# Kernel tuning notes

Hardware: AMD Instinct MI355X
Metric: run time of the kernel (lower is better)

Reference implementation:

```python
import jax, jax.numpy as jnp
import numpy as np

N = 100000      # nodes
E = 1600000     # edges (avg degree 16)
EL = 200000     # supervision (label) edges
D_IN, D_HID, D_OUT = 128, 128, 64


def setup_inputs() -> dict:
    key = jax.random.key(0)
    k = jax.random.split(key, 6)
    x = jax.random.normal(k[0], (N, D_IN), jnp.float32)
    edge_index = jax.random.randint(k[1], (2, E), 0, N, dtype=jnp.int32)
    edge_label_index = jax.random.randint(k[2], (2, EL), 0, N, dtype=jnp.int32)
    W1 = jax.random.normal(k[3], (D_IN, D_HID), jnp.float32) * (1.0 / np.sqrt(D_IN))
    b1 = jnp.zeros((D_HID,), jnp.float32)
    W2 = jax.random.normal(k[4], (D_HID, D_OUT), jnp.float32) * (1.0 / np.sqrt(D_HID))
    b2 = jnp.zeros((D_OUT,), jnp.float32)
    return {"x": x, "edge_index": edge_index, "edge_label_index": edge_label_index,
            "W1": W1, "b1": b1, "W2": W2, "b2": b2}


def gcn_layer(x, src, dst, W, b, n):
    """PyG-style GCNConv: linear -> sym-normalized scatter-add with self loops -> +bias."""
    h = x @ W                                   # [N, F]
    ones = jnp.ones(src.shape[0], h.dtype)
    deg = jax.ops.segment_sum(ones, dst, num_segments=n) + 1.0   # in-degree + self loop
    dinv = jax.lax.rsqrt(deg)                   # deg^{-1/2}
    norm = dinv[src] * dinv[dst]                # per-edge norm
    agg = jax.ops.segment_sum(h[src] * norm[:, None], dst, num_segments=n)
    agg = agg + h * (1.0 / deg)[:, None]        # self-loop contribution: dinv[i]^2
    return agg + b


def reference(x, edge_index, edge_label_index, W1, b1, W2, b2):
    src, dst = edge_index[0], edge_index[1]
    z = gcn_layer(x, src, dst, W1, b1, N)
    z = jax.nn.relu(z)                          # dropout omitted (eval mode)
    z = gcn_layer(z, src, dst, W2, b2, N)
    # decode: gather-dot over supervision edges
    return (z[edge_label_index[0]] * z[edge_label_index[1]]).sum(axis=-1)
```

## Files before the change

### kernel.cpp

```cpp
#include <hip/hip_runtime.h>
#include <stdint.h>

typedef __bf16 bf16x8 __attribute__((ext_vector_type(8)));
typedef float  floatx4 __attribute__((ext_vector_type(4)));
typedef float  floatx2 __attribute__((ext_vector_type(2)));
typedef __fp16 h2 __attribute__((ext_vector_type(2)));

__device__ __forceinline__ unsigned short f2b(float x){
    unsigned u = __float_as_uint(x);
    u = u + 0x7FFFu + ((u >> 16) & 1u);
    return (unsigned short)(u >> 16);
}
__device__ __forceinline__ float b2f(unsigned short h){
    return __uint_as_float(((unsigned)h) << 16);
}
__device__ __forceinline__ unsigned char f2f8(float x){
    int p = __builtin_amdgcn_cvt_pk_fp8_f32(x, x, 0, false);
    return (unsigned char)(p & 0xff);
}

__global__ __launch_bounds__(256) void k_scatter2(const int* __restrict__ src,
                                                  const int* __restrict__ dst,
                                                  int* __restrict__ gcur,
                                                  unsigned* __restrict__ slab,
                                                  int E_, int nbins){
    __shared__ int h[1024];
    __shared__ unsigned wbuf[4096];
    __shared__ unsigned short bbuf[4096];
    int t = threadIdx.x, blk = blockIdx.x;
    for (int i = t; i < nbins; i += 256) h[i] = 0;
    __syncthreads();
    int base = blk * 4096;
    int valid = E_ - base; if (valid > 4096) valid = 4096;
    #pragma unroll
    for (int j = 0; j < 4; j++){
        int li = (j * 256 + t) * 4;
        int e = base + li;
        if (e < E_){
            int4 d = *(const int4*)(dst + e);
            int4 s = *(const int4*)(src + e);
            wbuf[li + 0] = ((unsigned)(d.x & 127) << 25) | (unsigned)s.x;
            wbuf[li + 1] = ((unsigned)(d.y & 127) << 25) | (unsigned)s.y;
            wbuf[li + 2] = ((unsigned)(d.z & 127) << 25) | (unsigned)s.z;
            wbuf[li + 3] = ((unsigned)(d.w & 127) << 25) | (unsigned)s.w;
            bbuf[li + 0] = (unsigned short)(d.x >> 7);
            bbuf[li + 1] = (unsigned short)(d.y >> 7);
            bbuf[li + 2] = (unsigned short)(d.z >> 7);
            bbuf[li + 3] = (unsigned short)(d.w >> 7);
            atomicAdd(&h[d.x >> 7], 1);
            atomicAdd(&h[d.y >> 7], 1);
            atomicAdd(&h[d.z >> 7], 1);
            atomicAdd(&h[d.w >> 7], 1);
        }
    }
    __syncthreads();
    for (int i = t; i < nbins; i += 256){
        int hv = h[i];
        h[i] = hv ? atomicAdd(&gcur[i], hv) : 0;
    }
    __syncthreads();
    for (int i = t; i < valid; i += 256){
        int bin = bbuf[i];
        int p = atomicAdd(&h[bin], 1);
        slab[(size_t)bin * 4096 + p] = wbuf[i];
    }
}

__global__ __launch_bounds__(256) void k_binsort(const unsigned* __restrict__ slab,
                                                 const int* __restrict__ gcur,
                                                 int* __restrict__ csr,
                                                 int* __restrict__ cnt,
                                                 int* __restrict__ off,
                                                 float* __restrict__ dinv,
                                                 int n, int nbins){
    int b = blockIdx.x, t = threadIdx.x;
    __shared__ int sv[1024], sp[256];
    #pragma unroll
    for (int k = 0; k < 4; k++){
        int i = t * 4 + k;
        sv[i] = (i < nbins) ? gcur[i] : 0;
    }
    __syncthreads();
    int a0 = sv[t * 4], a1 = sv[t * 4 + 1], a2 = sv[t * 4 + 2], a3 = sv[t * 4 + 3];
    sp[t] = a0 + a1 + a2 + a3;
    __syncthreads();
    for (int o = 1; o < 256; o <<= 1){
        int v = (t >= o) ? sp[t - o] : 0;
        __syncthreads();
        sp[t] += v;
        __syncthreads();
    }
    int basep = t ? sp[t - 1] : 0;
    sv[t * 4]     = basep;
    sv[t * 4 + 1] = basep + a0;
    sv[t * 4 + 2] = basep + a0 + a1;
    sv[t * 4 + 3] = basep + a0 + a1 + a2;
    __syncthreads();
    int s0 = sv[b];
    int len = gcur[b];
    if (len > 4096) len = 4096;
    const unsigned* seg = slab + (size_t)b * 4096;
    __shared__ int cl[128], sc[128], cur[128];
    __shared__ unsigned buf[4096], outb[4096];
    if (t < 128){ cl[t] = 0; cur[t] = 0; }
    __syncthreads();
    for (int i = t; i < len; i += 256) buf[i] = seg[i];
    __syncthreads();
    for (int i = t; i < len; i += 256) atomicAdd(&cl[buf[i] >> 25], 1);
    __syncthreads();
    if (t < 128) sc[t] = cl[t];
    __syncthreads();
    for (int o = 1; o < 128; o <<= 1){
        int v = 0;
        if (t < 128 && t >= o) v = sc[t - o];
        __syncthreads();
        if (t < 128) sc[t] += v;
        __syncthreads();
    }
    for (int i = t; i < len; i += 256){
        unsigned w = buf[i];
        int nd = (int)(w >> 25);
        int p = (sc[nd] - cl[nd]) + atomicAdd(&cur[nd], 1);
        outb[p] = w & 0x1FFFFFFu;
    }
    __syncthreads();
    for (int i = t; i < len; i += 256) csr[s0 + i] = (int)outb[i];
    if (t < 128){
        int node = b * 128 + t;
        if (node < n){
            cnt[node] = cl[t];
            off[node] = s0 + (sc[t] - cl[t]);
            dinv[node] = rsqrtf((float)cl[t] + 1.0f);
        }
    }
}

__global__ __launch_bounds__(256) void k_init(const float* __restrict__ W1,
                                              const float* __restrict__ W2,
                                              unsigned short* __restrict__ wf1,
                                              unsigned* __restrict__ w2p,
                                              int* __restrict__ gcur, int nbins){
    int blk = blockIdx.x, t = threadIdx.x;
    if (blk == 24){
        for (int i = t; i < nbins; i += 256) gcur[i] = 0;
        return;
    }
    int f = blk * 256 + t;
    if (f < 2048){
        int lane = f & 63;
        int ctkc = f >> 6;
        int kc = ctkc & 3, ct = ctkc >> 2;
        int col = ct * 16 + (lane & 15);
        int k0  = kc * 32 + (lane >> 4) * 8;
        unsigned short* d = wf1 + (size_t)f * 8;
        #pragma unroll
        for (int j = 0; j < 8; j++) d[j] = f2b(W1[(k0 + j) * 128 + col]);
    } else if (f < 2048 + 4096){
        int lf = f - 2048;
        int kp = lf >> 6, lane = lf & 63;
        h2 p = __builtin_amdgcn_cvt_pkrtz(W2[(2 * kp) * 64 + lane],
                                          W2[(2 * kp + 1) * 64 + lane]);
        w2p[lf] = __builtin_bit_cast(unsigned, p);
    }
}

__global__ __launch_bounds__(256) void k_gemm1(const float* __restrict__ x,
                                               const unsigned short* __restrict__ wf,
                                               const float* __restrict__ dinv,
                                               unsigned char* __restrict__ hs, int n){
    __shared__ unsigned short Wl[16384];
    __shared__ unsigned short Al[64 * 136];
    int t = threadIdx.x;
    long rowBase = (long)blockIdx.x * 64;
    {
        const uint4* s4 = (const uint4*)wf;
        uint4* d4 = (uint4*)Wl;
        #pragma unroll
        for (int i = 0; i < 8; i++) d4[t + i * 256] = s4[t + i * 256];
    }
    {
        const float4* xs = (const float4*)(x + rowBase * 128);
        #pragma unroll
        for (int k = 0; k < 8; k++){
            int i = t + k * 256;
            int r = i >> 5, c4 = (i & 31) << 2;
            float4 v = make_float4(0.f, 0.f, 0.f, 0.f);
            if (rowBase + r < n) v = xs[i];
            unsigned lo = (unsigned)f2b(v.x) | ((unsigned)f2b(v.y) << 16);
            unsigned hi = (unsigned)f2b(v.z) | ((unsigned)f2b(v.w) << 16);
            *(uint2*)&Al[r * 136 + c4] = make_uint2(lo, hi);
        }
    }
    __syncthreads();
    int w = t >> 6, lane = t & 63, lr = lane & 15, q = lane >> 4;
    floatx4 zero = {0.f, 0.f, 0.f, 0.f};
    floatx4 acc[8];
    #pragma unroll
    for (int ct = 0; ct < 8; ct++) acc[ct] = zero;
    #pragma unroll
    for (int kc = 0; kc < 4; kc++){
        bf16x8 af = *(const bf16x8*)&Al[(w * 16 + lr) * 136 + kc * 32 + q * 8];
        #pragma unroll
        for (int ct = 0; ct < 8; ct++){
            bf16x8 bf = *(const bf16x8*)&Wl[((ct * 4 + kc) * 64 + lane) * 8];
            acc[ct] = __builtin_amdgcn_mfma_f32_16x16x32_bf16(af, bf, acc[ct], 0, 0, 0);
        }
    }
    long r0 = rowBase + w * 16 + q * 4;
    #pragma unroll
    for (int r = 0; r < 4; r++){
        long row = r0 + r;
        if (row >= n) continue;
        float dv = dinv[row];
        unsigned char* orow = hs + row * 128 + lr;
        #pragma unroll
        for (int ct = 0; ct < 8; ct++) orow[ct * 16] = f2f8(acc[ct][r] * dv);
    }
}

__global__ __launch_bounds__(256) void k_agg1g2(const unsigned char* __restrict__ hs,
                                                const int* __restrict__ off,
                                                const int* __restrict__ cnt,
                                                const int* __restrict__ csr,
                                                const float* __restrict__ dinv,
                                                const float* __restrict__ b1,
                                                const unsigned* __restrict__ w2p,
                                                unsigned short* __restrict__ hs2,
                                                int n, int nwaves){
    __shared__ unsigned W2l[4096];
    __shared__ unsigned zp[4][64];
    int t = threadIdx.x;
    {
        const uint4* w4 = (const uint4*)w2p;
        uint4* d4 = (uint4*)W2l;
        #pragma unroll
        for (int i = 0; i < 4; i++) d4[t + i * 256] = w4[t + i * 256];
    }
    __syncthreads();
    int wband = t >> 6, lane = t & 63;
    float2 bb = ((const float2*)b1)[lane];
    for (int wid = blockIdx.x * 4 + wband; wid < n; wid += nwaves){
        size_t i = (size_t)wid;
        int start = off[wid], c = cnt[wid];
        unsigned short v0 = *(const unsigned short*)(hs + i * 128 + lane * 2);
        floatx2 f0 = __builtin_amdgcn_cvt_pk_f32_fp8((int)v0, false);
        float a0 = f0.x, a1 = f0.y;
        int j = 0;
        for (; j + 8 <= c; j += 8){
            size_t s0 = (size_t)csr[start + j + 0];
            size_t s1 = (size_t)csr[start + j + 1];
            size_t s2 = (size_t)csr[start + j + 2];
            size_t s3 = (size_t)csr[start + j + 3];
            size_t s4 = (size_t)csr[start + j + 4];
            size_t s5 = (size_t)csr[start + j + 5];
            size_t s6 = (size_t)csr[start + j + 6];
            size_t s7 = (size_t)csr[start + j + 7];
            unsigned short w0 = *(const unsigned short*)(hs + s0 * 128 + lane * 2);
            unsigned short w1 = *(const unsigned short*)(hs + s1 * 128 + lane * 2);
            unsigned short w2 = *(const unsigned short*)(hs + s2 * 128 + lane * 2);
            unsigned short w3 = *(const unsigned short*)(hs + s3 * 128 + lane * 2);
            unsigned short w4 = *(const unsigned short*)(hs + s4 * 128 + lane * 2);
            unsigned short w5 = *(const unsigned short*)(hs + s5 * 128 + lane * 2);
            unsigned short w6 = *(const unsigned short*)(hs + s6 * 128 + lane * 2);
            unsigned short w7 = *(const unsigned short*)(hs + s7 * 128 + lane * 2);
            floatx2 g0 = __builtin_amdgcn_cvt_pk_f32_fp8((int)w0, false);
            floatx2 g1 = __builtin_amdgcn_cvt_pk_f32_fp8((int)w1, false);
            floatx2 g2 = __builtin_amdgcn_cvt_pk_f32_fp8((int)w2, false);
            floatx2 g3 = __builtin_amdgcn_cvt_pk_f32_fp8((int)w3, false);
            floatx2 g4 = __builtin_amdgcn_cvt_pk_f32_fp8((int)w4, false);
            floatx2 g5 = __builtin_amdgcn_cvt_pk_f32_fp8((int)w5, false);
            floatx2 g6 = __builtin_amdgcn_cvt_pk_f32_fp8((int)w6, false);
            floatx2 g7 = __builtin_amdgcn_cvt_pk_f32_fp8((int)w7, false);
            a0 += g0.x; a1 += g0.y;
            a0 += g1.x; a1 += g1.y;
            a0 += g2.x; a1 += g2.y;
            a0 += g3.x; a1 += g3.y;
            a0 += g4.x; a1 += g4.y;
            a0 += g5.x; a1 += g5.y;
            a0 += g6.x; a1 += g6.y;
            a0 += g7.x; a1 += g7.y;
        }
        for (; j < c; j++){
            size_t s = (size_t)csr[start + j];
            unsigned short v = *(const unsigned short*)(hs + s * 128 + lane * 2);
            floatx2 g = __builtin_amdgcn_cvt_pk_f32_fp8((int)v, false);
            a0 += g.x; a1 += g.y;
        }
        float dv = dinv[wid];
        float z0 = fmaxf(fmaf(dv, a0, bb.x), 0.f);
        float z1 = fmaxf(fmaf(dv, a1, bb.y), 0.f);
        zp[wband][lane] = __builtin_bit_cast(unsigned, __builtin_amdgcn_cvt_pkrtz(z0, z1));
        float acc0 = 0.f, acc1 = 0.f;
        #pragma unroll 8
        for (int kp = 0; kp < 64; kp += 2){
            h2 wa = __builtin_bit_cast(h2, W2l[kp * 64 + lane]);
            h2 wb = __builtin_bit_cast(h2, W2l[(kp + 1) * 64 + lane]);
            h2 za = __builtin_bit_cast(h2, zp[wband][kp]);
            h2 zb = __builtin_bit_cast(h2, zp[wband][kp + 1]);
            acc0 = __builtin_amdgcn_fdot2(za, wa, acc0, false);
            acc1 = __builtin_amdgcn_fdot2(zb, wb, acc1, false);
        }
        hs2[i * 64 + lane] = f2b((acc0 + acc1) * dv);
    }
}

__global__ __launch_bounds__(256) void k_agg2(const unsigned short* __restrict__ hs,
                                              const int* __restrict__ off,
                                              const int* __restrict__ cnt,
                                              const int* __restrict__ csr,
                                              const float* __restrict__ dinv,
                                              const float* __restrict__ b,
                                              unsigned short* __restrict__ z, int n){
    int wv = (blockIdx.x * 256 + threadIdx.x) >> 6;
    int lane = threadIdx.x & 63;
    int half = lane >> 5, hl = lane & 31;
    int node = wv * 2 + half;
    if (node >= n) return;
    size_t i = (size_t)node;
    int start = off[node], c = cnt[node];
    unsigned v0 = *(const unsigned*)(hs + i * 64 + hl * 2);
    float a0 = b2f((unsigned short)v0);
    float a1 = b2f((unsigned short)(v0 >> 16));
    int j = 0;
    for (; j + 8 <= c; j += 8){
        size_t s0 = (size_t)csr[start + j + 0];
        size_t s1 = (size_t)csr[start + j + 1];
        size_t s2 = (size_t)csr[start + j + 2];
        size_t s3 = (size_t)csr[start + j + 3];
        size_t s4 = (size_t)csr[start + j + 4];
        size_t s5 = (size_t)csr[start + j + 5];
        size_t s6 = (size_t)csr[start + j + 6];
        size_t s7 = (size_t)csr[start + j + 7];
        unsigned w0 = *(const unsigned*)(hs + s0 * 64 + hl * 2);
        unsigned w1 = *(const unsigned*)(hs + s1 * 64 + hl * 2);
        unsigned w2 = *(const unsigned*)(hs + s2 * 64 + hl * 2);
        unsigned w3 = *(const unsigned*)(hs + s3 * 64 + hl * 2);
        unsigned w4 = *(const unsigned*)(hs + s4 * 64 + hl * 2);
        unsigned w5 = *(const unsigned*)(hs + s5 * 64 + hl * 2);
        unsigned w6 = *(const unsigned*)(hs + s6 * 64 + hl * 2);
        unsigned w7 = *(const unsigned*)(hs + s7 * 64 + hl * 2);
        a0 += b2f((unsigned short)w0); a1 += b2f((unsigned short)(w0 >> 16));
        a0 += b2f((unsigned short)w1); a1 += b2f((unsigned short)(w1 >> 16));
        a0 += b2f((unsigned short)w2); a1 += b2f((unsigned short)(w2 >> 16));
        a0 += b2f((unsigned short)w3); a1 += b2f((unsigned short)(w3 >> 16));
        a0 += b2f((unsigned short)w4); a1 += b2f((unsigned short)(w4 >> 16));
        a0 += b2f((unsigned short)w5); a1 += b2f((unsigned short)(w5 >> 16));
        a0 += b2f((unsigned short)w6); a1 += b2f((unsigned short)(w6 >> 16));
        a0 += b2f((unsigned short)w7); a1 += b2f((unsigned short)(w7 >> 16));
    }
    for (; j < c; j++){
        size_t s = (size_t)csr[start + j];
        unsigned v = *(const unsigned*)(hs + s * 64 + hl * 2);
        a0 += b2f((unsigned short)v);
        a1 += b2f((unsigned short)(v >> 16));
    }
    float dv = dinv[node];
    float2 bb = ((const float2*)b)[hl];
    float r0 = fmaf(dv, a0, bb.x);
    float r1 = fmaf(dv, a1, bb.y);
    *(unsigned*)(z + i * 64 + hl * 2) = (unsigned)f2b(r0) | ((unsigned)f2b(r1) << 16);
}

__global__ __launch_bounds__(256) void k_decode(const unsigned short* __restrict__ z,
                                                const int* __restrict__ es,
                                                const int* __restrict__ et,
                                                float* __restrict__ out, int m){
    int wv = (blockIdx.x * 256 + threadIdx.x) >> 6;
    int lane = threadIdx.x & 63;
    int e = wv * 4 + (lane >> 4);
    int ql = lane & 15;
    float p = 0.f;
    if (e < m){
        size_t s = (size_t)es[e], t2 = (size_t)et[e];
        uint2 vs = *(const uint2*)(z + s * 64 + ql * 4);
        uint2 vt = *(const uint2*)(z + t2 * 64 + ql * 4);
        p = b2f((unsigned short)vs.x) * b2f((unsigned short)vt.x)
          + b2f((unsigned short)(vs.x >> 16)) * b2f((unsigned short)(vt.x >> 16))
          + b2f((unsigned short)vs.y) * b2f((unsigned short)vt.y)
          + b2f((unsigned short)(vs.y >> 16)) * b2f((unsigned short)(vt.y >> 16));
    }
    #pragma unroll
    for (int o = 8; o > 0; o >>= 1) p += __shfl_xor(p, o);
    if (ql == 0 && e < m) out[e] = p;
}


extern "C" void kernel_launch(void* const* d_in, const int* in_sizes, int n_in,
                              void* d_out, int out_size, void* d_ws, size_t ws_size,
                              hipStream_t stream){
    const float* x   = (const float*)d_in[0];
    const int*   ei  = (const int*)d_in[1];
    const int*   eli = (const int*)d_in[2];
    const float* W1  = (const float*)d_in[3];
    const float* b1  = (const float*)d_in[4];
    const float* W2  = (const float*)d_in[5];
    const float* b2  = (const float*)d_in[6];
    float* out = (float*)d_out;

    int N_  = in_sizes[0] / 128;
    int E_  = in_sizes[1] / 2;
    int EL_ = in_sizes[2] / 2;
    int NBINS = (N_ + 127) >> 7;
    const int EPB = 4096;
    int NBLK = (E_ + EPB - 1) / EPB;

    char* w = (char*)d_ws;
    size_t o = 0;
    auto alloc = [&](size_t bytes) -> size_t {
        size_t r = o; o += (bytes + 511) & ~(size_t)511; return r;
    };
    size_t o_cnt  = alloc((size_t)N_ * 4);
    size_t o_off  = alloc((size_t)N_ * 4);
    size_t o_dinv = alloc((size_t)N_ * 4);
    size_t o_gcur = alloc((size_t)NBINS * 4);
    size_t o_csr  = alloc((size_t)E_ * 4);
    size_t o_wf1  = alloc(16384 * 2);
    size_t o_w2p  = alloc(4096 * 4);
    size_t o_slab = alloc((size_t)NBINS * 4096 * 4);
    size_t o_hs1  = alloc((size_t)N_ * 128);
    size_t o_hs2  = alloc((size_t)N_ * 64 * 2);

    int* cnt  = (int*)(w + o_cnt);
    int* off  = (int*)(w + o_off);
    float* dinv = (float*)(w + o_dinv);
    int* gcur = (int*)(w + o_gcur);
    int* csr  = (int*)(w + o_csr);
    unsigned short* wf1 = (unsigned short*)(w + o_wf1);
    unsigned* w2p = (unsigned*)(w + o_w2p);
    unsigned* slab = (unsigned*)(w + o_slab);
    unsigned char* hs1 = (unsigned char*)(w + o_hs1);
    unsigned short* hs2 = (unsigned short*)(w + o_hs2);
    unsigned short* z2  = (unsigned short*)(w + o_slab);

    const int AGG1_BLOCKS = 2048;
    int nwaves = AGG1_BLOCKS * 4;

    k_init    <<<25, 256, 0, stream>>>(W1, W2, wf1, w2p, gcur, NBINS);
    k_scatter2<<<NBLK, 256, 0, stream>>>(ei, ei + E_, gcur, slab, E_, NBINS);
    k_binsort <<<NBINS, 256, 0, stream>>>(slab, gcur, csr, cnt, off, dinv, N_, NBINS);
    k_gemm1   <<<(N_ + 63) / 64, 256, 0, stream>>>(x, wf1, dinv, hs1, N_);
    k_agg1g2  <<<AGG1_BLOCKS, 256, 0, stream>>>(hs1, off, cnt, csr, dinv, b1, w2p, hs2, N_, nwaves);
    k_agg2    <<<(N_ + 7) / 8, 256, 0, stream>>>(hs2, off, cnt, csr, dinv, b2, z2, N_);
    k_decode  <<<(EL_ + 15) / 16, 256, 0, stream>>>(z2, eli, eli + EL_, out, EL_);
}
```

Baseline: 270.2 us.

## Gather 8 neighbor rows per wave with 16-byte loads in both aggregations

Both aggregation kernels now split the wavefront into 8 groups of 8 lanes. Each group loads a whole neighbor row with 16-byte vector loads, so 8 neighbors are in flight per instruction, and the partial sums are combined with cross-lane shuffles. This replaces the narrow 2- and 4-byte per-lane gathers, meaning fewer memory instructions and more memory-level parallelism. In exchange, each lane holds more accumulator registers and the kernels pay for the shuffle reduction. k_agg2 now runs one node per wave instead of two, so its grid doubles.

Measured after the change: 301.6 us. +11.6%, slower.

```diff
diff --git a/kernel.cpp b/kernel.cpp
--- a/kernel.cpp
+++ b/kernel.cpp
@@ -18,6 +18,25 @@
     int p = __builtin_amdgcn_cvt_pk_fp8_f32(x, x, 0, false);
     return (unsigned char)(p & 0xff);
 }
+
+#define ACC16(v) do{ \
+    floatx2 p; \
+    p = __builtin_amdgcn_cvt_pk_f32_fp8((int)(v).x, false); acc[0]+=p.x;  acc[1]+=p.y;  \
+    p = __builtin_amdgcn_cvt_pk_f32_fp8((int)(v).x, true ); acc[2]+=p.x;  acc[3]+=p.y;  \
+    p = __builtin_amdgcn_cvt_pk_f32_fp8((int)(v).y, false); acc[4]+=p.x;  acc[5]+=p.y;  \
+    p = __builtin_amdgcn_cvt_pk_f32_fp8((int)(v).y, true ); acc[6]+=p.x;  acc[7]+=p.y;  \
+    p = __builtin_amdgcn_cvt_pk_f32_fp8((int)(v).z, false); acc[8]+=p.x;  acc[9]+=p.y;  \
+    p = __builtin_amdgcn_cvt_pk_f32_fp8((int)(v).z, true ); acc[10]+=p.x; acc[11]+=p.y; \
+    p = __builtin_amdgcn_cvt_pk_f32_fp8((int)(v).w, false); acc[12]+=p.x; acc[13]+=p.y; \
+    p = __builtin_amdgcn_cvt_pk_f32_fp8((int)(v).w, true ); acc[14]+=p.x; acc[15]+=p.y; \
+}while(0)
+
+#define ACC8(v) do{ \
+    acc[0]+=b2f((unsigned short)(v).x); acc[1]+=b2f((unsigned short)((v).x>>16)); \
+    acc[2]+=b2f((unsigned short)(v).y); acc[3]+=b2f((unsigned short)((v).y>>16)); \
+    acc[4]+=b2f((unsigned short)(v).z); acc[5]+=b2f((unsigned short)((v).z>>16)); \
+    acc[6]+=b2f((unsigned short)(v).w); acc[7]+=b2f((unsigned short)((v).w>>16)); \
+}while(0)
 
 __global__ __launch_bounds__(256) void k_scatter2(const int* __restrict__ src,
                                                   const int* __restrict__ dst,
@@ -238,58 +257,72 @@
     }
     __syncthreads();
     int wband = t >> 6, lane = t & 63;
-    float2 bb = ((const float2*)b1)[lane];
+    int g = lane >> 3, q = lane & 7;
+    float4 bbl = ((const float4*)b1)[q * 4 + 0];
+    float4 bbh = ((const float4*)b1)[q * 4 + 1];
+    float4 bbl2 = ((const float4*)b1)[q * 4 + 2];
+    float4 bbh2 = ((const float4*)b1)[q * 4 + 3];
     for (int wid = blockIdx.x * 4 + wband; wid < n; wid += nwaves){
         size_t i = (size_t)wid;
         int start = off[wid], c = cnt[wid];
-        unsigned short v0 = *(const unsigned short*)(hs + i * 128 + lane * 2);
-        floatx2 f0 = __builtin_amdgcn_cvt_pk_f32_fp8((int)v0, false);
-        float a0 = f0.x, a1 = f0.y;
+        float acc[16];
+        #pragma unroll
+        for (int k2 = 0; k2 < 16; k2++) acc[k2] = 0.f;
         int j = 0;
+        for (; j + 16 <= c; j += 16){
+            int r0 = csr[start + j + g];
+            int r1 = csr[start + j + 8 + g];
+            uint4 v0 = *(const uint4*)(hs + (size_t)r0 * 128 + q * 16);
+            uint4 v1 = *(const uint4*)(hs + (size_t)r1 * 128 + q * 16);
+            ACC16(v0);
+            ACC16(v1);
+        }
         for (; j + 8 <= c; j += 8){
-            size_t s0 = (size_t)csr[start + j + 0];
-            size_t s1 = (size_t)csr[start + j + 1];
-            size_t s2 = (size_t)csr[start + j + 2];
-            size_t s3 = (size_t)csr[start + j + 3];
-            size_t s4 = (size_t)csr[start + j + 4];
-            size_t s5 = (size_t)csr[start + j + 5];
-            size_t s6 = (size_t)csr[start + j + 6];
-            size_t s7 = (size_t)csr[start + j + 7];
-            unsigned short w0 = *(const unsigned short*)(hs + s0 * 128 + lane * 2);
-            unsigned short w1 = *(const unsigned short*)(hs + s1 * 128 + lane * 2);
-            unsigned short w2 = *(const unsigned short*)(hs + s2 * 128 + lane * 2);
-            unsigned short w3 = *(const unsigned short*)(hs + s3 * 128 + lane * 2);
-            unsigned short w4 = *(const unsigned short*)(hs + s4 * 128 + lane * 2);
-            unsigned short w5 = *(const unsigned short*)(hs + s5 * 128 + lane * 2);
-            unsigned short w6 = *(const unsigned short*)(hs + s6 * 128 + lane * 2);
-            unsigned short w7 = *(const unsigned short*)(hs + s7 * 128 + lane * 2);
-            floatx2 g0 = __builtin_amdgcn_cvt_pk_f32_fp8((int)w0, false);
-            floatx2 g1 = __builtin_amdgcn_cvt_pk_f32_fp8((int)w1, false);
-            floatx2 g2 = __builtin_amdgcn_cvt_pk_f32_fp8((int)w2, false);
-            floatx2 g3 = __builtin_amdgcn_cvt_pk_f32_fp8((int)w3, false);
-            floatx2 g4 = __builtin_amdgcn_cvt_pk_f32_fp8((int)w4, false);
-            floatx2 g5 = __builtin_amdgcn_cvt_pk_f32_fp8((int)w5, false);
-            floatx2 g6 = __builtin_amdgcn_cvt_pk_f32_fp8((int)w6, false);
-            floatx2 g7 = __builtin_amdgcn_cvt_pk_f32_fp8((int)w7, false);
-            a0 += g0.x; a1 += g0.y;
-            a0 += g1.x; a1 += g1.y;
-            a0 += g2.x; a1 += g2.y;
-            a0 += g3.x; a1 += g3.y;
-            a0 += g4.x; a1 += g4.y;
-            a0 += g5.x; a1 += g5.y;
-            a0 += g6.x; a1 += g6.y;
-            a0 += g7.x; a1 += g7.y;
-        }
-        for (; j < c; j++){
-            size_t s = (size_t)csr[start + j];
-            unsigned short v = *(const unsigned short*)(hs + s * 128 + lane * 2);
-            floatx2 g = __builtin_amdgcn_cvt_pk_f32_fp8((int)v, false);
-            a0 += g.x; a1 += g.y;
+            int r0 = csr[start + j + g];
+            uint4 v0 = *(const uint4*)(hs + (size_t)r0 * 128 + q * 16);
+            ACC16(v0);
+        }
+        int rem = c - j;
+        if (rem > 0){
+            int gg = (g < rem) ? g : 0;
+            int r0 = csr[start + j + gg];
+            uint4 v0 = *(const uint4*)(hs + (size_t)r0 * 128 + q * 16);
+            if (g < rem){ ACC16(v0); }
+        }
+        #pragma unroll
+        for (int k2 = 0; k2 < 16; k2++){
+            acc[k2] += __shfl_xor(acc[k2], 8);
+            acc[k2] += __shfl_xor(acc[k2], 16);
+            acc[k2] += __shfl_xor(acc[k2], 32);
+        }
+        {
+            uint4 sv2 = *(const uint4*)(hs + i * 128 + q * 16);
+            ACC16(sv2);
         }
         float dv = dinv[wid];
-        float z0 = fmaxf(fmaf(dv, a0, bb.x), 0.f);
-        float z1 = fmaxf(fmaf(dv, a1, bb.y), 0.f);
-        zp[wband][lane] = __builtin_bit_cast(unsigned, __builtin_amdgcn_cvt_pkrtz(z0, z1));
+        float z[16];
+        z[0]  = fmaxf(fmaf(dv, acc[0],  bbl.x), 0.f);
+        z[1]  = fmaxf(fmaf(dv, acc[1],  bbl.y), 0.f);
+        z[2]  = fmaxf(fmaf(dv, acc[2],  bbl.z), 0.f);
+        z[3]  = fmaxf(fmaf(dv, acc[3],  bbl.w), 0.f);
+        z[4]  = fmaxf(fmaf(dv, acc[4],  bbh.x), 0.f);
+        z[5]  = fmaxf(fmaf(dv, acc[5],  bbh.y), 0.f);
+        z[6]  = fmaxf(fmaf(dv, acc[6],  bbh.z), 0.f);
+        z[7]  = fmaxf(fmaf(dv, acc[7],  bbh.w), 0.f);
+        z[8]  = fmaxf(fmaf(dv, acc[8],  bbl2.x), 0.f);
+        z[9]  = fmaxf(fmaf(dv, acc[9],  bbl2.y), 0.f);
+        z[10] = fmaxf(fmaf(dv, acc[10], bbl2.z), 0.f);
+        z[11] = fmaxf(fmaf(dv, acc[11], bbl2.w), 0.f);
+        z[12] = fmaxf(fmaf(dv, acc[12], bbh2.x), 0.f);
+        z[13] = fmaxf(fmaf(dv, acc[13], bbh2.y), 0.f);
+        z[14] = fmaxf(fmaf(dv, acc[14], bbh2.z), 0.f);
+        z[15] = fmaxf(fmaf(dv, acc[15], bbh2.w), 0.f);
+        if (g == 0){
+            #pragma unroll
+            for (int m = 0; m < 8; m++)
+                zp[wband][q * 8 + m] = __builtin_bit_cast(unsigned,
+                    __builtin_amdgcn_cvt_pkrtz(z[2 * m], z[2 * m + 1]));
+        }
         float acc0 = 0.f, acc1 = 0.f;
         #pragma unroll 8
         for (int kp = 0; kp < 64; kp += 2){
@@ -311,54 +344,57 @@
                                               const float* __restrict__ dinv,
                                               const float* __restrict__ b,
                                               unsigned short* __restrict__ z, int n){
-    int wv = (blockIdx.x * 256 + threadIdx.x) >> 6;
+    int node = (blockIdx.x * 256 + threadIdx.x) >> 6;
     int lane = threadIdx.x & 63;
-    int half = lane >> 5, hl = lane & 31;
-    int node = wv * 2 + half;
     if (node >= n) return;
+    int g = lane >> 3, q = lane & 7;
     size_t i = (size_t)node;
     int start = off[node], c = cnt[node];
-    unsigned v0 = *(const unsigned*)(hs + i * 64 + hl * 2);
-    float a0 = b2f((unsigned short)v0);
-    float a1 = b2f((unsigned short)(v0 >> 16));
+    float4 bbl = ((const float4*)b)[q * 2];
+    float4 bbh = ((const float4*)b)[q * 2 + 1];
+    float acc[8];
+    #pragma unroll
+    for (int k2 = 0; k2 < 8; k2++) acc[k2] = 0.f;
     int j = 0;
+    for (; j + 16 <= c; j += 16){
+        int r0 = csr[start + j + g];
+        int r1 = csr[start + j + 8 + g];
+        uint4 v0 = *(const uint4*)(hs + (size_t)r0 * 64 + q * 8);
+        uint4 v1 = *(const uint4*)(hs + (size_t)r1 * 64 + q * 8);
+        ACC8(v0);
+        ACC8(v1);
+    }
     for (; j + 8 <= c; j += 8){
-        size_t s0 = (size_t)csr[start + j + 0];
-        size_t s1 = (size_t)csr[start + j + 1];
-        size_t s2 = (size_t)csr[start + j + 2];
-        size_t s3 = (size_t)csr[start + j + 3];
-        size_t s4 = (size_t)csr[start + j + 4];
-        size_t s5 = (size_t)csr[start + j + 5];
-        size_t s6 = (size_t)csr[start + j + 6];
-        size_t s7 = (size_t)csr[start + j + 7];
-        unsigned w0 = *(const unsigned*)(hs + s0 * 64 + hl * 2);
-        unsigned w1 = *(const unsigned*)(hs + s1 * 64 + hl * 2);
-        unsigned w2 = *(const unsigned*)(hs + s2 * 64 + hl * 2);
-        unsigned w3 = *(const unsigned*)(hs + s3 * 64 + hl * 2);
-        unsigned w4 = *(const unsigned*)(hs + s4 * 64 + hl * 2);
-        unsigned w5 = *(const unsigned*)(hs + s5 * 64 + hl * 2);
-        unsigned w6 = *(const unsigned*)(hs + s6 * 64 + hl * 2);
-        unsigned w7 = *(const unsigned*)(hs + s7 * 64 + hl * 2);
-        a0 += b2f((unsigned short)w0); a1 += b2f((unsigned short)(w0 >> 16));
-        a0 += b2f((unsigned short)w1); a1 += b2f((unsigned short)(w1 >> 16));
-        a0 += b2f((unsigned short)w2); a1 += b2f((unsigned short)(w2 >> 16));
-        a0 += b2f((unsigned short)w3); a1 += b2f((unsigned short)(w3 >> 16));
-        a0 += b2f((unsigned short)w4); a1 += b2f((unsigned short)(w4 >> 16));
-        a0 += b2f((unsigned short)w5); a1 += b2f((unsigned short)(w5 >> 16));
-        a0 += b2f((unsigned short)w6); a1 += b2f((unsigned short)(w6 >> 16));
-        a0 += b2f((unsigned short)w7); a1 += b2f((unsigned short)(w7 >> 16));
-    }
-    for (; j < c; j++){
-        size_t s = (size_t)csr[start + j];
-        unsigned v = *(const unsigned*)(hs + s * 64 + hl * 2);
-        a0 += b2f((unsigned short)v);
-        a1 += b2f((unsigned short)(v >> 16));
+        int r0 = csr[start + j + g];
+        uint4 v0 = *(const uint4*)(hs + (size_t)r0 * 64 + q * 8);
+        ACC8(v0);
+    }
+    int rem = c - j;
+    if (rem > 0){
+        int gg = (g < rem) ? g : 0;
+        int r0 = csr[start + j + gg];
+        uint4 v0 = *(const uint4*)(hs + (size_t)r0 * 64 + q * 8);
+        if (g < rem){ ACC8(v0); }
+    }
+    #pragma unroll
+    for (int k2 = 0; k2 < 8; k2++){
+        acc[k2] += __shfl_xor(acc[k2], 8);
+        acc[k2] += __shfl_xor(acc[k2], 16);
+        acc[k2] += __shfl_xor(acc[k2], 32);
+    }
+    {
+        uint4 sv2 = *(const uint4*)(hs + i * 64 + q * 8);
+        ACC8(sv2);
     }
     float dv = dinv[node];
-    float2 bb = ((const float2*)b)[hl];
-    float r0 = fmaf(dv, a0, bb.x);
-    float r1 = fmaf(dv, a1, bb.y);
-    *(unsigned*)(z + i * 64 + hl * 2) = (unsigned)f2b(r0) | ((unsigned)f2b(r1) << 16);
+    if (g == 0){
+        uint4 o;
+        o.x = (unsigned)f2b(fmaf(dv, acc[0], bbl.x)) | ((unsigned)f2b(fmaf(dv, acc[1], bbl.y)) << 16);
+        o.y = (unsigned)f2b(fmaf(dv, acc[2], bbl.z)) | ((unsigned)f2b(fmaf(dv, acc[3], bbl.w)) << 16);
+        o.z = (unsigned)f2b(fmaf(dv, acc[4], bbh.x)) | ((unsigned)f2b(fmaf(dv, acc[5], bbh.y)) << 16);
+        o.w = (unsigned)f2b(fmaf(dv, acc[6], bbh.z)) | ((unsigned)f2b(fmaf(dv, acc[7], bbh.w)) << 16);
+        *(uint4*)(z + i * 64 + q * 8) = o;
+    }
 }
 
 __global__ __launch_bounds__(256) void k_decode(const unsigned short* __restrict__ z,
@@ -440,6 +476,6 @@
     k_binsort <<<NBINS, 256, 0, stream>>>(slab, gcur, csr, cnt, off, dinv, N_, NBINS);
     k_gemm1   <<<(N_ + 63) / 64, 256, 0, stream>>>(x, wf1, dinv, hs1, N_);
     k_agg1g2  <<<AGG1_BLOCKS, 256, 0, stream>>>(hs1, off, cnt, csr, dinv, b1, w2p, hs2, N_, nwaves);
-    k_agg2    <<<(N_ + 7) / 8, 256, 0, stream>>>(hs2, off, cnt, csr, dinv, b2, z2, N_);
+    k_agg2    <<<(N_ + 3) / 4, 256, 0, stream>>>(hs2, off, cnt, csr, dinv, b2, z2, N_);
     k_decode  <<<(EL_ + 15) / 16, 256, 0, stream>>>(z2, eli, eli + EL_, out, EL_);
 }
```
